# Kernel optimization log

Measured on AMD Instinct MI355X. Metric: run time of the kernel, lower is better.

Reference implementation:

```python
import jax, jax.numpy as jnp
import numpy as np

TEMPERATURE = 1.0
NEG = -1e9
EPS = 1e-8


def setup_inputs() -> dict:
    key = jax.random.key(0)
    k1, k2, k3 = jax.random.split(key, 3)
    B, H = 524288, 32
    scores = jax.random.normal(k1, (B, H), dtype=jnp.float32)
    rankings = jax.random.randint(k2, (B, H), 0, 33, dtype=jnp.int32)
    mask = jax.random.randint(k3, (B, H), 0, 2, dtype=jnp.int32).astype(bool)
    return {"scores": scores, "rankings": rankings, "mask": mask}


def reference(scores, rankings, mask):
    B, H = scores.shape
    # effective validity: horse present AND has a ranking > 0 (top_k=None)
    m = mask & (rankings > 0)
    # masked, temperature-scaled scores; -1e9 entries underflow to exactly 0 in softmax
    s = jnp.where(m, scores / TEMPERATURE, NEG)
    p = jax.nn.softmax(s, axis=1)  # [B, H], ~0 at invalid slots

    n_valid = jnp.sum(m, axis=1)  # [B]
    # ideal order: valid horses sorted by ranking ascending (invalid pushed to end)
    rank_key = jnp.where(m, rankings, jnp.iinfo(jnp.int32).max)
    rank_order = jnp.argsort(rank_key, axis=1)          # stable sort
    # prediction order: valid horses in original index order (matches torch.where)
    pos_order = jnp.argsort(~m, axis=1)                 # stable: valid first

    q = jnp.take_along_axis(p, rank_order, axis=1)      # ideal_probs, aligned by list position
    pr = jnp.take_along_axis(p, pos_order, axis=1)      # pred_probs,  aligned by list position

    # positions >= n_valid are padding
    valid_pos = jnp.arange(H)[None, :] < n_valid[:, None]
    q_safe = jnp.where(valid_pos, q, 1.0)
    pr_safe = jnp.where(valid_pos, pr, 1.0)
    # KL(ideal || pred) with the original's log(pred + 1e-8)
    kl_terms = q_safe * (jnp.log(q_safe) - jnp.log(pr_safe + EPS))
    kl = jnp.sum(jnp.where(valid_pos, kl_terms, 0.0), axis=1)  # [B]

    # rows with <= 1 valid ranked horse are skipped entirely
    row_ok = n_valid > 1
    n_rows = jnp.maximum(jnp.sum(row_ok), 1)
    return jnp.sum(jnp.where(row_ok, kl, 0.0)) / n_rows  # reduction='mean'
```

## Files before the change

kernel.cpp:

```cpp
#include <hip/hip_runtime.h>
#include <stdint.h>


__global__ __launch_bounds__(256) void listwise_kernel(
    const float* __restrict__ scores,
    const int* __restrict__ rankings,
    const unsigned char* __restrict__ mask_u8,
    float* __restrict__ ws_kl,
    int* __restrict__ ws_cnt,
    int npairs)
{
    const int lane = threadIdx.x & 63;
    const int gl   = lane & 31;
    const int sh   = lane & 32;
    const uint32_t lmask = (1u << gl) - 1u;
    const int wid = threadIdx.x >> 6;
    const int wavesPerBlock = blockDim.x >> 6;
    const int gw = blockIdx.x * wavesPerBlock + wid;
    const int totWaves = gridDim.x * wavesPerBlock;

    unsigned char probe = mask_u8[lane];
    const bool mask_is_i32 =
        (__ballot(((lane & 3) != 0) && (probe != 0)) == 0ull);
    const int* mask_i32 = (const int*)mask_u8;

    float th_kl = 0.0f;
    int   th_cnt = 0;

    for (int pair = gw; pair < npairs; pair += totWaves) {
        const int base = pair * 64 + lane;
        const float s = scores[base];
        const int   r = rankings[base];
        const int   mk = mask_is_i32 ? mask_i32[base] : (int)mask_u8[base];
        const bool valid = (mk != 0) && (r > 0);

        const unsigned long long balv = __ballot(valid);
        const uint32_t vm = (uint32_t)(balv >> sh);
        const int nv = __popc(vm);

        float x = valid ? s : -3.0e38f;
        #pragma unroll
        for (int m = 16; m >= 1; m >>= 1) x = fmaxf(x, __shfl_xor(x, m));
        const float e = valid ? __expf(s - x) : 0.0f;
        float se = e;
        #pragma unroll
        for (int m = 16; m >= 1; m >>= 1) se += __shfl_xor(se, m);
        const float p = e / se;
        const float lp1 = __logf(p);
        const float lp2 = __logf(p + 1e-8f);

        const uint32_t v = ((uint32_t)(r - 1)) & 31u;
        uint32_t E = vm;
        int c_lt = 0;
        #pragma unroll
        for (int i = 4; i >= 0; --i) {
            const unsigned long long bb = __ballot((v >> i) & 1u);
            const uint32_t bi = (uint32_t)(bb >> sh);
            const uint32_t t = (v >> i) & 1u;
            c_lt += t ? __popc(E & ~bi) : 0;
            E &= t ? bi : ~bi;
        }
        const int eq_below = __popc(E & lmask);
        const int j_rank = c_lt + eq_below;
        const int j_pos  = __popc(vm & lmask);

        const int inv_pos = gl - j_pos;
        const int dst = valid ? j_pos : (nv + inv_pos);
        const int scat = __builtin_amdgcn_ds_permute((sh + dst) << 2,
                                                     __float_as_int(lp2));
        const int gidx = valid ? j_rank : 0;
        const float g = __int_as_float(
            __builtin_amdgcn_ds_bpermute((sh + gidx) << 2, scat));

        float term = valid ? p * (lp1 - g) : 0.0f;
        #pragma unroll
        for (int m = 16; m >= 1; m >>= 1) term += __shfl_xor(term, m);

        if (gl == 0 && nv > 1) { th_kl += term; th_cnt += 1; }
    }

    #pragma unroll
    for (int m = 32; m >= 1; m >>= 1) {
        th_kl  += __shfl_xor(th_kl, m);
        th_cnt += __shfl_xor(th_cnt, m);
    }
    __shared__ float s_kl[8];
    __shared__ int   s_cnt[8];
    if (lane == 0) { s_kl[wid] = th_kl; s_cnt[wid] = th_cnt; }
    __syncthreads();
    if (threadIdx.x == 0) {
        float k = 0.0f; int c = 0;
        for (int i = 0; i < wavesPerBlock; ++i) { k += s_kl[i]; c += s_cnt[i]; }
        atomicAdd(ws_kl, k);
        atomicAdd(ws_cnt, c);
    }
}

__global__ void finalize_kernel(const float* __restrict__ ws_kl,
                                const int* __restrict__ ws_cnt,
                                float* __restrict__ out)
{
    if (threadIdx.x == 0) {
        int c = *ws_cnt;
        if (c < 1) c = 1;
        out[0] = *ws_kl / (float)c;
    }
}

extern "C" void kernel_launch(void* const* d_in, const int* in_sizes, int n_in,
                              void* d_out, int out_size, void* d_ws, size_t ws_size,
                              hipStream_t stream) {
    const float* scores = (const float*)d_in[0];
    const int* rankings = (const int*)d_in[1];
    const unsigned char* mask = (const unsigned char*)d_in[2];
    float* out = (float*)d_out;

    const int total = in_sizes[0];
    const int npairs = total / 64;

    float* wsf = (float*)d_ws;
    int*   wsi = (int*)d_ws;

    hipMemsetAsync(d_ws, 0, 8, stream);

    const int threads = 256;
    const int blocks = 2048;
    listwise_kernel<<<blocks, threads, 0, stream>>>(
        scores, rankings, mask, wsf, wsi + 1, npairs);

    finalize_kernel<<<1, 64, 0, stream>>>(wsf, wsi + 1, out);
}
```

Before: 237.8 us.

## Rewrite listwise KL as one thread per row with algebraic log-ratio

Replaces the half-wavefront-per-row design, which relied on ballots, shuffles and permutes, with one thread per row. Each thread loads its row through vector loads, builds sort keys, and computes each horse's rank position by counting smaller keys (O(H^2) compares). It compacts valid scores into a padded LDS row for the gather. The KL is computed algebraically as sum(e_i*(s_i - s_j))/sum(e_i), which avoids per-element logs and the divide. This drops the max subtraction and the 1e-8 epsilon, so the result can drift slightly and could overflow for large scores. It trades cross-lane traffic for more per-thread registers and ALU work, and the 33 KB LDS per block may limit occupancy.

```diff
diff --git a/kernel.cpp b/kernel.cpp
--- a/kernel.cpp
+++ b/kernel.cpp
@@ -2,81 +2,111 @@
 #include <stdint.h>
 
 
-__global__ __launch_bounds__(256) void listwise_kernel(
+#define H 32
+
+__global__ __launch_bounds__(256, 4) void listwise_kernel(
     const float* __restrict__ scores,
     const int* __restrict__ rankings,
     const unsigned char* __restrict__ mask_u8,
     float* __restrict__ ws_kl,
     int* __restrict__ ws_cnt,
-    int npairs)
+    int nrows)
 {
-    const int lane = threadIdx.x & 63;
-    const int gl   = lane & 31;
-    const int sh   = lane & 32;
-    const uint32_t lmask = (1u << gl) - 1u;
-    const int wid = threadIdx.x >> 6;
-    const int wavesPerBlock = blockDim.x >> 6;
-    const int gw = blockIdx.x * wavesPerBlock + wid;
-    const int totWaves = gridDim.x * wavesPerBlock;
+    __shared__ float lds_row[256 * 33];
+    __shared__ float s_kl[4];
+    __shared__ int   s_cnt[4];
+
+    const int tid  = threadIdx.x;
+    const int lane = tid & 63;
+    const int wid  = tid >> 6;
+    const int row  = blockIdx.x * 256 + tid;
 
     unsigned char probe = mask_u8[lane];
     const bool mask_is_i32 =
         (__ballot(((lane & 3) != 0) && (probe != 0)) == 0ull);
-    const int* mask_i32 = (const int*)mask_u8;
 
     float th_kl = 0.0f;
     int   th_cnt = 0;
 
-    for (int pair = gw; pair < npairs; pair += totWaves) {
-        const int base = pair * 64 + lane;
-        const float s = scores[base];
-        const int   r = rankings[base];
-        const int   mk = mask_is_i32 ? mask_i32[base] : (int)mask_u8[base];
-        const bool valid = (mk != 0) && (r > 0);
+    if (row < nrows) {
+        float s[H];
+        {
+            const float4* p = (const float4*)(scores + (size_t)row * H);
+            #pragma unroll
+            for (int c = 0; c < H / 4; ++c) {
+                float4 v = p[c];
+                s[4*c+0] = v.x; s[4*c+1] = v.y; s[4*c+2] = v.z; s[4*c+3] = v.w;
+            }
+        }
+        int r[H];
+        {
+            const int4* p = (const int4*)(rankings + (size_t)row * H);
+            #pragma unroll
+            for (int c = 0; c < H / 4; ++c) {
+                int4 v = p[c];
+                r[4*c+0] = v.x; r[4*c+1] = v.y; r[4*c+2] = v.z; r[4*c+3] = v.w;
+            }
+        }
 
-        const unsigned long long balv = __ballot(valid);
-        const uint32_t vm = (uint32_t)(balv >> sh);
-        const int nv = __popc(vm);
+        uint32_t vbits = 0;
+        if (mask_is_i32) {
+            const int4* p = (const int4*)((const int*)mask_u8 + (size_t)row * H);
+            #pragma unroll
+            for (int c = 0; c < H / 4; ++c) {
+                int4 v = p[c];
+                vbits |= (v.x != 0 ? 1u : 0u) << (4*c+0);
+                vbits |= (v.y != 0 ? 1u : 0u) << (4*c+1);
+                vbits |= (v.z != 0 ? 1u : 0u) << (4*c+2);
+                vbits |= (v.w != 0 ? 1u : 0u) << (4*c+3);
+            }
+        } else {
+            const uint4* p = (const uint4*)(mask_u8 + (size_t)row * H);
+            #pragma unroll
+            for (int c = 0; c < 2; ++c) {
+                uint4 v = p[c];
+                uint32_t w[4] = {v.x, v.y, v.z, v.w};
+                #pragma unroll
+                for (int q = 0; q < 4; ++q)
+                    #pragma unroll
+                    for (int b = 0; b < 4; ++b)
+                        vbits |= ((((w[q] >> (8*b)) & 0xFFu) != 0u) ? 1u : 0u)
+                                 << (16*c + 4*q + b);
+            }
+        }
 
-        float x = valid ? s : -3.0e38f;
+        uint32_t key[H];
+        int nv = 0;
         #pragma unroll
-        for (int m = 16; m >= 1; m >>= 1) x = fmaxf(x, __shfl_xor(x, m));
-        const float e = valid ? __expf(s - x) : 0.0f;
-        float se = e;
+        for (int k = 0; k < H; ++k) {
+            const bool valid = (((vbits >> k) & 1u) != 0u) && (r[k] > 0);
+            key[k] = valid ? ((((uint32_t)r[k]) << 5) | (uint32_t)k)
+                           : (0x10000u | (uint32_t)k);
+            nv += valid ? 1 : 0;
+        }
+
+        float* rowp = &lds_row[tid * 33];
+        int jp = 0;
         #pragma unroll
-        for (int m = 16; m >= 1; m >>= 1) se += __shfl_xor(se, m);
-        const float p = e / se;
-        const float lp1 = __logf(p);
-        const float lp2 = __logf(p + 1e-8f);
+        for (int k = 0; k < H; ++k) {
+            const bool valid = key[k] < 0x10000u;
+            rowp[valid ? jp : 32] = s[k];
+            jp += valid ? 1 : 0;
+        }
 
-        const uint32_t v = ((uint32_t)(r - 1)) & 31u;
-        uint32_t E = vm;
-        int c_lt = 0;
+        float se = 0.0f, num = 0.0f;
         #pragma unroll
-        for (int i = 4; i >= 0; --i) {
-            const unsigned long long bb = __ballot((v >> i) & 1u);
-            const uint32_t bi = (uint32_t)(bb >> sh);
-            const uint32_t t = (v >> i) & 1u;
-            c_lt += t ? __popc(E & ~bi) : 0;
-            E &= t ? bi : ~bi;
+        for (int i = 0; i < H; ++i) {
+            int j = 0;
+            #pragma unroll
+            for (int k = 0; k < H; ++k) j += (key[k] < key[i]) ? 1 : 0;
+            const float g = rowp[j];
+            const float e = __expf(s[i]);
+            const bool valid = key[i] < 0x10000u;
+            se += valid ? e : 0.0f;
+            const float t = e * (s[i] - g);
+            num += valid ? t : 0.0f;
         }
-        const int eq_below = __popc(E & lmask);
-        const int j_rank = c_lt + eq_below;
-        const int j_pos  = __popc(vm & lmask);
-
-        const int inv_pos = gl - j_pos;
-        const int dst = valid ? j_pos : (nv + inv_pos);
-        const int scat = __builtin_amdgcn_ds_permute((sh + dst) << 2,
-                                                     __float_as_int(lp2));
-        const int gidx = valid ? j_rank : 0;
-        const float g = __int_as_float(
-            __builtin_amdgcn_ds_bpermute((sh + gidx) << 2, scat));
-
-        float term = valid ? p * (lp1 - g) : 0.0f;
-        #pragma unroll
-        for (int m = 16; m >= 1; m >>= 1) term += __shfl_xor(term, m);
-
-        if (gl == 0 && nv > 1) { th_kl += term; th_cnt += 1; }
+        if (nv > 1) { th_kl = __fdividef(num, se); th_cnt = 1; }
     }
 
     #pragma unroll
@@ -84,15 +114,11 @@
         th_kl  += __shfl_xor(th_kl, m);
         th_cnt += __shfl_xor(th_cnt, m);
     }
-    __shared__ float s_kl[8];
-    __shared__ int   s_cnt[8];
     if (lane == 0) { s_kl[wid] = th_kl; s_cnt[wid] = th_cnt; }
     __syncthreads();
-    if (threadIdx.x == 0) {
-        float k = 0.0f; int c = 0;
-        for (int i = 0; i < wavesPerBlock; ++i) { k += s_kl[i]; c += s_cnt[i]; }
-        atomicAdd(ws_kl, k);
-        atomicAdd(ws_cnt, c);
+    if (tid == 0) {
+        atomicAdd(ws_kl,  s_kl[0] + s_kl[1] + s_kl[2] + s_kl[3]);
+        atomicAdd(ws_cnt, s_cnt[0] + s_cnt[1] + s_cnt[2] + s_cnt[3]);
     }
 }
 
@@ -116,7 +142,7 @@
     float* out = (float*)d_out;
 
     const int total = in_sizes[0];
-    const int npairs = total / 64;
+    const int nrows = total / H;
 
     float* wsf = (float*)d_ws;
     int*   wsi = (int*)d_ws;
@@ -124,9 +150,9 @@
     hipMemsetAsync(d_ws, 0, 8, stream);
 
     const int threads = 256;
-    const int blocks = 2048;
+    const int blocks = (nrows + threads - 1) / threads;
     listwise_kernel<<<blocks, threads, 0, stream>>>(
-        scores, rankings, mask, wsf, wsi + 1, npairs);
+        scores, rankings, mask, wsf, wsi + 1, nrows);
 
     finalize_kernel<<<1, 64, 0, stream>>>(wsf, wsi + 1, out);
 }
```

Result: faster. 216.5 us (-9.0%).
